# Kernel optimization log

Hardware: AMD Instinct MI355X
Metric: run time of the kernel (lower is better)

## Reference

```python
import jax, jax.numpy as jnp
import numpy as np

D_MODEL = 1024
N_HEADS = 16
D_FF = 2 * D_MODEL
EPS = 1e-6


def setup_inputs() -> dict:
    key = jax.random.key(0)
    ks = jax.random.split(key, 12)
    B, S, D = 2, 2048, D_MODEL
    w = lambda k, shape: (jax.random.normal(k, shape, dtype=jnp.float32) * 0.02)
    return {
        "x": jax.random.normal(ks[0], (B, S, D), dtype=jnp.float32),
        "mask": jnp.ones((B, S, S), dtype=jnp.int32),
        "alpha1": jnp.ones((D,), jnp.float32),
        "bias1": jnp.zeros((D,), jnp.float32),
        "Wq": w(ks[1], (D, D)), "bq": jnp.zeros((D,), jnp.float32),
        "Wk": w(ks[2], (D, D)), "bk": jnp.zeros((D,), jnp.float32),
        "Wv": w(ks[3], (D, D)), "bv": jnp.zeros((D,), jnp.float32),
        "Wo": w(ks[4], (D, D)), "bo": jnp.zeros((D,), jnp.float32),
        "alpha2": jnp.ones((D,), jnp.float32),
        "bias2": jnp.zeros((D,), jnp.float32),
        "W1": w(ks[5], (D, D_FF)), "b1": jnp.zeros((D_FF,), jnp.float32),
        "W2": w(ks[6], (D_FF, D)), "b2": jnp.zeros((D,), jnp.float32),
    }


def _norm(x, alpha, bias):
    # torch: alpha*(x-mean)/(std+eps)+bias, std is unbiased (ddof=1)
    mu = jnp.mean(x, axis=-1, keepdims=True)
    sd = jnp.std(x, axis=-1, ddof=1, keepdims=True)
    return alpha * (x - mu) / (sd + EPS) + bias


def _gelu(x):
    return jax.nn.gelu(x, approximate=False)  # torch F.gelu exact


def _attention(x2, mask, Wq, bq, Wk, bk, Wv, bv, Wo, bo):
    B, S, D = x2.shape
    h, dk = N_HEADS, D // N_HEADS
    # project and split heads: [B, h, S, dk]
    q = (x2 @ Wq + bq).reshape(B, S, h, dk).transpose(0, 2, 1, 3)
    k = (x2 @ Wk + bk).reshape(B, S, h, dk).transpose(0, 2, 1, 3)
    v = (x2 @ Wv + bv).reshape(B, S, h, dk).transpose(0, 2, 1, 3)
    scores = jnp.einsum('bhqd,bhkd->bhqk', q, k) / np.sqrt(dk).astype(np.float32)
    scores = jnp.where(mask[:, None] == 0, jnp.float32(-1e9), scores)
    attn = jax.nn.softmax(scores, axis=-1)
    out = jnp.einsum('bhqk,bhkd->bhqd', attn, v)
    out = out.transpose(0, 2, 1, 3).reshape(B, S, D)
    return out @ Wo + bo


def reference(x, mask, alpha1, bias1, Wq, bq, Wk, bk, Wv, bv, Wo, bo,
              alpha2, bias2, W1, b1, W2, b2):
    x2 = _norm(x, alpha1, bias1)
    x = x + _attention(x2, mask, Wq, bq, Wk, bk, Wv, bv, Wo, bo)
    x2 = _norm(x, alpha2, bias2)
    ff = _gelu(_gelu(x2 @ W1 + b1) @ W2 + b2)
    return x + ff
```

## Files before the change

### kernel.cpp

```cpp
#include <hip/hip_runtime.h>
#include <math.h>

typedef __attribute__((ext_vector_type(8))) short v8s;
typedef __attribute__((ext_vector_type(4))) float v4f;
typedef __attribute__((ext_vector_type(2))) float v2f;
typedef __attribute__((ext_vector_type(16))) float v16f;
typedef __attribute__((ext_vector_type(4))) unsigned int v4u;
typedef __attribute__((ext_vector_type(2))) unsigned int v2u;

#define MFMA16(a,b,c) __builtin_amdgcn_mfma_f32_16x16x32_bf16(a,b,c,0,0,0)
#define MFMA32(a,b,c) __builtin_amdgcn_mfma_f32_32x32x16_bf16(a,b,c,0,0,0)
#define QSCALE 0.18033688011112042f
#define MFIX   12.0f

typedef const __attribute__((address_space(1))) void* gp1_t;
typedef __attribute__((address_space(3))) void* lp3_t;
__device__ __forceinline__ void gll16(const void* g, void* l){
  __builtin_amdgcn_global_load_lds((gp1_t)g, (lp3_t)l, 16, 0, 0);
}
#define VMCNT(n) asm volatile("s_waitcnt vmcnt(" #n ")" ::: "memory")

__device__ __forceinline__ unsigned short f2b(float f){
  unsigned u = __builtin_bit_cast(unsigned, f);
  u += 0x7FFFu + ((u>>16)&1u);
  return (unsigned short)(u>>16);
}
__device__ __forceinline__ float b2f(unsigned short u){
  return __builtin_bit_cast(float, ((unsigned)u)<<16);
}
__device__ __forceinline__ unsigned cvtpk(float lo, float hi){
  unsigned r;
  asm("v_cvt_pk_bf16_f32 %0, %1, %2" : "=v"(r) : "v"(lo), "v"(hi));
  return r;
}
__device__ __forceinline__ float gelu_exact(float x){
  return 0.5f*x*(1.0f + erff(x*0.70710678118654752f));
}

__global__ __launch_bounds__(256) void ln_kernel(const float* __restrict__ x,
    const float* __restrict__ alpha, const float* __restrict__ bias,
    unsigned short* __restrict__ out)
{
  const int D = 1024;
  int row = blockIdx.x;
  int tid = threadIdx.x;
  const float* xr = x + (size_t)row*D;
  v4f v = ((const v4f*)xr)[tid];
  float s  = v[0]+v[1]+v[2]+v[3];
  float s2 = v[0]*v[0]+v[1]*v[1]+v[2]*v[2]+v[3]*v[3];
  #pragma unroll
  for (int off=1; off<64; off<<=1){ s += __shfl_xor(s, off); s2 += __shfl_xor(s2, off); }
  __shared__ float red[8];
  int w = tid>>6;
  if ((tid&63)==0){ red[w]=s; red[4+w]=s2; }
  __syncthreads();
  s  = red[0]+red[1]+red[2]+red[3];
  s2 = red[4]+red[5]+red[6]+red[7];
  float mu  = s*(1.0f/D);
  float var = (s2 - (float)D*mu*mu)*(1.0f/(D-1));
  float inv = 1.0f/(sqrtf(fmaxf(var,0.0f)) + 1e-6f);
  v4f a  = ((const v4f*)alpha)[tid];
  v4f bi = ((const v4f*)bias)[tid];
  unsigned short o[4];
  #pragma unroll
  for (int i=0;i<4;i++) o[i] = f2b(a[i]*(v[i]-mu)*inv + bi[i]);
  v2u pk; pk[0] = (unsigned)o[0] | ((unsigned)o[1]<<16);
          pk[1] = (unsigned)o[2] | ((unsigned)o[3]<<16);
  ((v2u*)(out + (size_t)row*D))[tid] = pk;
}

__global__ __launch_bounds__(256) void preprocess(
    const float* __restrict__ Wq, const float* __restrict__ Wk,
    const float* __restrict__ Wv, const float* __restrict__ Wo,
    const float* __restrict__ W1, const float* __restrict__ W2,
    const int* __restrict__ mask, const float* __restrict__ x,
    const float* __restrict__ alpha1, const float* __restrict__ bias1,
    unsigned short* __restrict__ wqkvT, unsigned short* __restrict__ woT,
    unsigned short* __restrict__ w1T, unsigned short* __restrict__ w2T,
    unsigned char* __restrict__ flags, unsigned short* __restrict__ x2b)
{
  __shared__ float t[32][33];
  __shared__ float red[8];
  __shared__ int f[4];
  int bid = blockIdx.x;
  int tid = threadIdx.x;
  if (bid < 8192){
    const float* in; unsigned short* out; int K, N, idx;
    if (bid < 3072){
      int m = bid >> 10; idx = bid & 1023;
      in = (m==0)?Wq:(m==1)?Wk:Wv; out = wqkvT + (size_t)m*1024*1024; K=1024; N=1024;
    } else if (bid < 4096){ idx = bid-3072; in=Wo; out=woT; K=1024; N=1024; }
    else if (bid < 6144){   idx = bid-4096; in=W1; out=w1T; K=1024; N=2048; }
    else {                  idx = bid-6144; in=W2; out=w2T; K=2048; N=1024; }
    int ntiles = N >> 5;
    int n0 = (idx % ntiles)*32, k0 = (idx / ntiles)*32;
    int tx = tid & 31, ty = tid >> 5;
    #pragma unroll
    for (int j=0;j<4;j++) t[ty+8*j][tx] = in[(size_t)(k0+ty+8*j)*N + n0+tx];
    __syncthreads();
    #pragma unroll
    for (int j=0;j<4;j++) out[(size_t)(n0+ty+8*j)*K + k0+tx] = f2b(t[tx][ty+8*j]);
  } else if (bid < 10240){
    const int S = 2048;
    int idx = bid - 8192;
    int kt = idx & 31, qt = (idx>>5)&31, b = idx>>10;
    const int* mp = mask + (size_t)b*S*S + (size_t)(qt*64)*S + kt*64;
    int ok = 1;
    #pragma unroll
    for (int i=0;i<16;i++){
      int e = tid + i*256;
      int row = e>>6, col = e&63;
      ok &= (mp[(size_t)row*S + col] != 0);
    }
    ok = __all(ok) ? 1 : 0;
    if ((tid&63)==0) f[tid>>6] = ok;
    __syncthreads();
    if (tid==0) flags[idx] = (unsigned char)(f[0]&f[1]&f[2]&f[3]);
  } else {
    const int D = 1024;
    int row = bid - 10240;
    const float* xr = x + (size_t)row*D;
    v4f v = ((const v4f*)xr)[tid];
    float s  = v[0]+v[1]+v[2]+v[3];
    float s2 = v[0]*v[0]+v[1]*v[1]+v[2]*v[2]+v[3]*v[3];
    #pragma unroll
    for (int off=1; off<64; off<<=1){ s += __shfl_xor(s, off); s2 += __shfl_xor(s2, off); }
    int w = tid>>6;
    if ((tid&63)==0){ red[w]=s; red[4+w]=s2; }
    __syncthreads();
    s  = red[0]+red[1]+red[2]+red[3];
    s2 = red[4]+red[5]+red[6]+red[7];
    float mu  = s*(1.0f/D);
    float var = (s2 - (float)D*mu*mu)*(1.0f/(D-1));
    float inv = 1.0f/(sqrtf(fmaxf(var,0.0f)) + 1e-6f);
    v4f a  = ((const v4f*)alpha1)[tid];
    v4f bi = ((const v4f*)bias1)[tid];
    unsigned short o[4];
    #pragma unroll
    for (int i=0;i<4;i++) o[i] = f2b(a[i]*(v[i]-mu)*inv + bi[i]);
    v2u pk; pk[0] = (unsigned)o[0] | ((unsigned)o[1]<<16);
            pk[1] = (unsigned)o[2] | ((unsigned)o[3]<<16);
    ((v2u*)(x2b + (size_t)row*D))[tid] = pk;
  }
}

__global__ __launch_bounds__(256) void gemm_qkv(
    const unsigned short* __restrict__ A, const unsigned short* __restrict__ Bt,
    const float* __restrict__ bq, const float* __restrict__ bk, const float* __restrict__ bv,
    unsigned short* __restrict__ qB, unsigned short* __restrict__ kB,
    unsigned short* __restrict__ vT)
{
  const int K = 1024, N = 1024;
  __shared__ unsigned short As[3][128][32];
  __shared__ unsigned short Bs[3][128][32];
  int m0 = blockIdx.x*128;
  int ny = blockIdx.y;
  int seg = ny>>3;
  int n0g = ny*128;
  int tid = threadIdx.x;
  int w = tid>>6, l = tid&63;
  int wm = (w>>1)*64, wn = (w&1)*64;
  int r16 = l&15, kq = l>>4;
  v4f acc[4][4] = {};
  int t4 = tid>>2, c8 = (tid&3)*8;
  const unsigned short* Ag = A  + (size_t)(m0 + t4)*K + c8;
  const unsigned short* Bg = Bt + (size_t)(n0g + t4)*K + c8;
  auto stageG = [&](int kb, int idx){
    char* a = (char*)&As[idx][0][0] + w*1024;
    char* b = (char*)&Bs[idx][0][0] + w*1024;
    gll16(Ag + kb,                a);
    gll16(Ag + (size_t)64*K + kb, a + 4096);
    gll16(Bg + kb,                b);
    gll16(Bg + (size_t)64*K + kb, b + 4096);
  };
  const int nk = K/32;
  stageG(0, 0); stageG(32, 1);
  for (int i=0; i<nk; i++){
    int cur = i%3;
    if (i+1 < nk) VMCNT(4); else VMCNT(0);
    __builtin_amdgcn_s_barrier();
    if (i+2 < nk) stageG((i+2)*32, (i+2)%3);
    v8s a[4], b[4];
    #pragma unroll
    for (int mi=0;mi<4;mi++) a[mi] = *(const v8s*)&As[cur][wm+mi*16+r16][kq*8];
    #pragma unroll
    for (int ni=0;ni<4;ni++) b[ni] = *(const v8s*)&Bs[cur][wn+ni*16+r16][kq*8];
    #pragma unroll
    for (int mi=0;mi<4;mi++)
      #pragma unroll
      for (int ni=0;ni<4;ni++)
        acc[mi][ni] = MFMA16(a[mi], b[ni], acc[mi][ni]);
  }
  int ncol0 = (ny&7)*128;
  if (seg < 2){
    unsigned short* ob = (seg==0) ? qB : kB;
    const float*    bp = (seg==0) ? bq : bk;
    float sc = (seg==0) ? QSCALE : 1.0f;
    #pragma unroll
    for (int mi=0;mi<4;mi++){
      #pragma unroll
      for (int ni=0;ni<4;ni++){
        int col = ncol0 + wn + ni*16 + r16;
        float bvv = bp[col];
        #pragma unroll
        for (int r=0;r<4;r++){
          int row = m0 + wm + mi*16 + kq*4 + r;
          ob[(size_t)row*N + col] = f2b((acc[mi][ni][r] + bvv)*sc);
        }
      }
    }
  } else {
    #pragma unroll
    for (int mi=0;mi<4;mi++){
      #pragma unroll
      for (int ni=0;ni<4;ni++){
        int col = ncol0 + wn + ni*16 + r16;
        int hh = col >> 6, dk = col & 63;
        float bvv = bv[col];
        int row = m0 + wm + mi*16 + kq*4;
        int bb = row >> 11, s = row & 2047;
        v2u pk;
        pk[0] = cvtpk(acc[mi][ni][0]+bvv, acc[mi][ni][1]+bvv);
        pk[1] = cvtpk(acc[mi][ni][2]+bvv, acc[mi][ni][3]+bvv);
        *(v2u*)(vT + ((size_t)(bb*16+hh)*64 + dk)*2048 + s) = pk;
      }
    }
  }
}

template<int MODE>
__global__ __launch_bounds__(256) void gemm64_bt(
    const unsigned short* __restrict__ A, const unsigned short* __restrict__ Bt,
    const float* __restrict__ bias, const float* __restrict__ res,
    unsigned short* __restrict__ outb, float* __restrict__ outf,
    int M, int N, int K)
{
  __shared__ unsigned short As[3][64][32];
  __shared__ unsigned short Bs[3][128][32];
  int m0 = blockIdx.x*64, n0 = blockIdx.y*128;
  int tid = threadIdx.x;
  int w = tid>>6, l = tid&63;
  int wm = (w>>1)*32, wn = (w&1)*64;
  int r16 = l&15, kq = l>>4;
  v4f acc[2][4] = {};
  int t4 = tid>>2, c8 = (tid&3)*8;
  const unsigned short* Ag = A  + (size_t)(m0 + t4)*K + c8;
  const unsigned short* Bg = Bt + (size_t)(n0 + t4)*K + c8;
  auto stageG = [&](int kb, int idx){
    char* a = (char*)&As[idx][0][0] + w*1024;
    char* b = (char*)&Bs[idx][0][0] + w*1024;
    gll16(Ag + kb,                a);
    gll16(Bg + kb,                b);
    gll16(Bg + (size_t)64*K + kb, b + 4096);
  };
  const int nk = K/32;
  stageG(0, 0); stageG(32, 1);
  for (int i=0; i<nk; i++){
    int cur = i%3;
    if (i+1 < nk) VMCNT(3); else VMCNT(0);
    __builtin_amdgcn_s_barrier();
    if (i+2 < nk) stageG((i+2)*32, (i+2)%3);
    v8s a[2], b[4];
    #pragma unroll
    for (int mi=0;mi<2;mi++) a[mi] = *(const v8s*)&As[cur][wm+mi*16+r16][kq*8];
    #pragma unroll
    for (int ni=0;ni<4;ni++) b[ni] = *(const v8s*)&Bs[cur][wn+ni*16+r16][kq*8];
    #pragma unroll
    for (int mi=0;mi<2;mi++)
      #pragma unroll
      for (int ni=0;ni<4;ni++)
        acc[mi][ni] = MFMA16(a[mi], b[ni], acc[mi][ni]);
  }
  #pragma unroll
  for (int mi=0;mi<2;mi++){
    #pragma unroll
    for (int ni=0;ni<4;ni++){
      int col = n0 + wn + ni*16 + r16;
      float bv = bias[col];
      #pragma unroll
      for (int r=0;r<4;r++){
        int row = m0 + wm + mi*16 + kq*4 + r;
        float t = acc[mi][ni][r] + bv;
        if (MODE==2 || MODE==3) t = gelu_exact(t);
        if (MODE==2) outb[(size_t)row*N + col] = f2b(t);
        else         outf[(size_t)row*N + col] = t + res[(size_t)row*N + col];
      }
    }
  }
}

__global__ __launch_bounds__(256, 4) void attn_kernel(
    const unsigned short* __restrict__ Q, const unsigned short* __restrict__ Kb,
    const unsigned short* __restrict__ vT, const int* __restrict__ mask,
    const unsigned char* __restrict__ flags,
    unsigned short* __restrict__ Opart, float* __restrict__ ml)
{
  const int S = 2048, D = 1024;
  __shared__ unsigned short Kb2[2][64][64];
  __shared__ unsigned short Vb2[2][64][64];
  int bid = (blockIdx.x & 7)*128 + (blockIdx.x >> 3);
  int half = bid & 1;
  int qt = (bid >> 1) & 15;
  int bh = bid >> 5;
  int b = bh >> 4, h = bh & 15;
  int tid = threadIdx.x, w = tid>>6, l = tid&63;
  int l31 = l & 31, hi = l >> 5;
  int pidx = (l ^ 32) << 2;
  const unsigned short* Qp  = Q  + (size_t)b*S*D + h*64;
  const unsigned short* Kp  = Kb + (size_t)b*S*D + h*64;
  const unsigned short* vTp = vT + (size_t)bh*64*S;
  int qrow = qt*128 + w*32 + l31;
  v8s qfr[4];
  #pragma unroll
  for (int ks=0;ks<4;ks++)
    qfr[ks] = *(const v8s*)(Qp + (size_t)qrow*D + ks*16 + hi*8);
  float l_run = 0.0f;
  v16f o0 = {}, o1 = {};
  const int* mp = mask + (size_t)b*S*S;
  const unsigned char* fl = flags + ((size_t)b*32 + qt*2)*32;
  int kt0 = half*16;
  unsigned long long okmask = __ballot( l < 16 ? ((fl[kt0+l] & fl[32+kt0+l]) != 0) : 1 );

  int srow = l>>3;
  int gsw  = (l&7) ^ srow;
  auto stage = [&](int ktg, int idx){
    int kt64 = ktg*64;
    #pragma unroll
    for (int sub=0; sub<2; sub++){
      int row = w*16 + sub*8 + srow;
      gll16(Kp  + (size_t)(kt64+row)*D + gsw*8, &Kb2[idx][w*16+sub*8][0]);
      gll16(vTp + (size_t)row*S + kt64 + gsw*8, &Vb2[idx][w*16+sub*8][0]);
    }
  };
  auto bfrag = [&](unsigned a0, unsigned a1, unsigned a4, unsigned a5) -> v8s {
    unsigned p0 = (unsigned)__builtin_amdgcn_ds_bpermute(pidx, (int)a0);
    unsigned p1 = (unsigned)__builtin_amdgcn_ds_bpermute(pidx, (int)a1);
    unsigned p4 = (unsigned)__builtin_amdgcn_ds_bpermute(pidx, (int)a4);
    unsigned p5 = (unsigned)__builtin_amdgcn_ds_bpermute(pidx, (int)a5);
    v4u pw;
    pw[0] = hi ? p4 : a0;
    pw[1] = hi ? p5 : a1;
    pw[2] = hi ? a4 : p0;
    pw[3] = hi ? a5 : p1;
    return __builtin_bit_cast(v8s, pw);
  };

  stage(kt0, 0);
  int cur = 0;
  for (int it=0; it<16; it++){
    __syncthreads();
    if (it+1 < 16) stage(kt0+it+1, cur^1);
    int ktg = kt0 + it;
    int l7 = l & 7;
    v16f s0 = {}, s1 = {};
    __builtin_amdgcn_s_setprio(1);
    #pragma unroll
    for (int ks=0; ks<4; ks++){
      v8s kf0 = *(const v8s*)&Kb2[cur][l31     ][(((ks*2) + hi) ^ l7)*8];
      v8s kf1 = *(const v8s*)&Kb2[cur][32 + l31][(((ks*2) + hi) ^ l7)*8];
      s0 = MFMA32(kf0, qfr[ks], s0);
      s1 = MFMA32(kf1, qfr[ks], s1);
    }
    __builtin_amdgcn_s_setprio(0);
    if (((~okmask) >> it) & 1ull){
      #pragma unroll
      for (int r=0;r<16;r++){
        int kvl = (r&3) + 8*(r>>2) + 4*hi;
        if (mp[(size_t)qrow*S + ktg*64 + kvl]      == 0) s0[r] = -3.0e38f;
        if (mp[(size_t)qrow*S + ktg*64 + 32 + kvl] == 0) s1[r] = -3.0e38f;
      }
    }
    #pragma unroll
    for (int r=0;r<16;r++){
      s0[r] = exp2f(s0[r] - MFIX);
      s1[r] = exp2f(s1[r] - MFIX);
    }
    float a0 = ((s0[0]+s0[1])+(s0[2]+s0[3])) + ((s0[4]+s0[5])+(s0[6]+s0[7]));
    float a1 = ((s0[8]+s0[9])+(s0[10]+s0[11])) + ((s0[12]+s0[13])+(s0[14]+s0[15]));
    float a2 = ((s1[0]+s1[1])+(s1[2]+s1[3])) + ((s1[4]+s1[5])+(s1[6]+s1[7]));
    float a3 = ((s1[8]+s1[9])+(s1[10]+s1[11])) + ((s1[12]+s1[13])+(s1[14]+s1[15]));
    float rs = (a0+a1) + (a2+a3);
    rs += __shfl_xor(rs, 32);
    l_run += rs;
    v8s pb0 = bfrag(cvtpk(s0[0],s0[1]),  cvtpk(s0[2],s0[3]),
                    cvtpk(s0[4],s0[5]),  cvtpk(s0[6],s0[7]));
    v8s pb1 = bfrag(cvtpk(s0[8],s0[9]),  cvtpk(s0[10],s0[11]),
                    cvtpk(s0[12],s0[13]),cvtpk(s0[14],s0[15]));
    v8s pb2 = bfrag(cvtpk(s1[0],s1[1]),  cvtpk(s1[2],s1[3]),
                    cvtpk(s1[4],s1[5]),  cvtpk(s1[6],s1[7]));
    v8s pb3 = bfrag(cvtpk(s1[8],s1[9]),  cvtpk(s1[10],s1[11]),
                    cvtpk(s1[12],s1[13]),cvtpk(s1[14],s1[15]));
    __builtin_amdgcn_s_setprio(1);
    #pragma unroll
    for (int kvs=0; kvs<4; kvs++){
      v8s pb = (kvs==0) ? pb0 : (kvs==1) ? pb1 : (kvs==2) ? pb2 : pb3;
      v8s vv0 = *(const v8s*)&Vb2[cur][l31     ][(((kvs*2) + hi) ^ l7)*8];
      v8s vv1 = *(const v8s*)&Vb2[cur][32 + l31][(((kvs*2) + hi) ^ l7)*8];
      o0 = MFMA32(vv0, pb, o0);
      o1 = MFMA32(vv1, pb, o1);
    }
    __builtin_amdgcn_s_setprio(0);
    cur ^= 1;
  }
  int rowg = b*S + qrow;
  unsigned short* Op = Opart + (size_t)half*4096*1024 + (size_t)rowg*1024 + h*64;
  #pragma unroll
  for (int p=0; p<8; p++){
    int dk = (p&1)*2 + 8*(p>>1) + 4*hi;
    *(unsigned*)(Op + dk)      = cvtpk(o0[2*p], o0[2*p+1]);
    *(unsigned*)(Op + 32 + dk) = cvtpk(o1[2*p], o1[2*p+1]);
  }
  if (!hi){
    float* mlp = ml + ((size_t)half*4096 + rowg)*32 + h*2;
    mlp[0] = l_run;
  }
}

__global__ __launch_bounds__(256) void attn_combine(const unsigned short* __restrict__ Opart,
    const float* __restrict__ ml, unsigned short* __restrict__ outB)
{
  int row = blockIdx.x;
  int t = threadIdx.x;
  int col = t*4;
  int head = col >> 6;
  float l1 = ml[(size_t)row*32 + head*2];
  float l2 = ml[((size_t)4096 + row)*32 + head*2];
  float inv = 1.0f / (l1 + l2);
  v2u au = *(const v2u*)(Opart + (size_t)row*1024 + col);
  v2u bu = *(const v2u*)(Opart + (size_t)4096*1024 + (size_t)row*1024 + col);
  float a0 = b2f((unsigned short)(au[0]&0xffff)), a1 = b2f((unsigned short)(au[0]>>16));
  float a2 = b2f((unsigned short)(au[1]&0xffff)), a3 = b2f((unsigned short)(au[1]>>16));
  float c0 = b2f((unsigned short)(bu[0]&0xffff)), c1 = b2f((unsigned short)(bu[0]>>16));
  float c2 = b2f((unsigned short)(bu[1]&0xffff)), c3 = b2f((unsigned short)(bu[1]>>16));
  v2u pk;
  pk[0] = cvtpk((a0 + c0)*inv, (a1 + c1)*inv);
  pk[1] = cvtpk((a2 + c2)*inv, (a3 + c3)*inv);
  *(v2u*)(outB + (size_t)row*1024 + col) = pk;
}

extern "C" void kernel_launch(void* const* d_in, const int* in_sizes, int n_in,
                              void* d_out, int out_size, void* d_ws, size_t ws_size,
                              hipStream_t stream)
{
  const int D=1024, DFF=2048, BS=4096;
  const float* x      = (const float*)d_in[0];
  const int*   mask   = (const int*)d_in[1];
  const float* alpha1 = (const float*)d_in[2];
  const float* bias1  = (const float*)d_in[3];
  const float* Wq     = (const float*)d_in[4];
  const float* bq     = (const float*)d_in[5];
  const float* Wk     = (const float*)d_in[6];
  const float* bk     = (const float*)d_in[7];
  const float* Wv     = (const float*)d_in[8];
  const float* bv     = (const float*)d_in[9];
  const float* Wo     = (const float*)d_in[10];
  const float* bo     = (const float*)d_in[11];
  const float* alpha2 = (const float*)d_in[12];
  const float* bias2  = (const float*)d_in[13];
  const float* W1     = (const float*)d_in[14];
  const float* b1     = (const float*)d_in[15];
  const float* W2     = (const float*)d_in[16];
  const float* b2     = (const float*)d_in[17];
  float* outp = (float*)d_out;

  char* ws = (char*)d_ws;
  size_t off = 0;
  auto alloc = [&](size_t bytes){ void* p = ws+off; off += (bytes+255)&~(size_t)255; return p; };
  unsigned short* x2b    = (unsigned short*)alloc((size_t)BS*D*2);
  unsigned short* qB     = (unsigned short*)alloc((size_t)BS*D*2);
  unsigned short* kB     = (unsigned short*)alloc((size_t)BS*D*2);
  unsigned short* vT     = (unsigned short*)alloc((size_t)BS*D*2);
  unsigned short* attnB  = (unsigned short*)alloc((size_t)BS*D*2);
  unsigned short* h1     = (unsigned short*)alloc((size_t)BS*DFF*2);
  float*          xres   = (float*)alloc((size_t)BS*D*4);
  unsigned short* wqkvT  = (unsigned short*)alloc((size_t)3*D*D*2);
  unsigned short* woT    = (unsigned short*)alloc((size_t)D*D*2);
  unsigned short* w1T    = (unsigned short*)alloc((size_t)D*DFF*2);
  unsigned short* w2T    = (unsigned short*)alloc((size_t)DFF*D*2);
  unsigned char*  flg    = (unsigned char*)alloc(2048);
  unsigned short* Opart  = (unsigned short*)alloc((size_t)2*BS*D*2);
  float*          mlbuf  = (float*)alloc((size_t)2*BS*16*2*4);

  preprocess<<<14336, 256, 0, stream>>>(Wq, Wk, Wv, Wo, W1, W2,
                                        mask, x, alpha1, bias1,
                                        wqkvT, woT, w1T, w2T, flg, x2b);

  gemm_qkv<<<dim3(BS/128, 24), 256, 0, stream>>>(x2b, wqkvT, bq, bk, bv, qB, kB, vT);

  attn_kernel<<<1024, 256, 0, stream>>>(qB, kB, vT, mask, flg, Opart, mlbuf);
  attn_combine<<<4096, 256, 0, stream>>>(Opart, mlbuf, attnB);

  gemm64_bt<1><<<dim3(BS/64, D/128), 256, 0, stream>>>(attnB, woT, bo, x, nullptr, xres, BS, D, D);

  ln_kernel<<<BS, 256, 0, stream>>>(xres, alpha2, bias2, x2b);

  gemm64_bt<2><<<dim3(BS/64, DFF/128), 256, 0, stream>>>(x2b, w1T, b1, nullptr, h1, nullptr, BS, DFF, D);
  gemm64_bt<3><<<dim3(BS/64, D/128), 256, 0, stream>>>(h1, w2T, b2, xres, nullptr, outp, BS, D, DFF);
}
```

Before: 249.7 us.

## Add triple-buffered BK=64 GEMM with async LDS loads for Wo and W2

Adds a new GEMM kernel for the two N=1024 output projections (attention Wo and FFN W2). It uses a K-tile of 64, a three-stage shared-memory ring filled by direct global-to-LDS loads, and an XOR swizzle to avoid bank conflicts. The aim is to hide global load latency and reduce barrier count per K step on the memory-bound, lower-occupancy projections. The cost is more LDS per block (about 72KB), which limits how many blocks fit per CU.

After: 238.0 us (median of 2 runs). 1.05x faster.

```diff
diff --git a/kernel.cpp b/kernel.cpp
--- a/kernel.cpp
+++ b/kernel.cpp
@@ -281,9 +281,77 @@
       for (int r=0;r<4;r++){
         int row = m0 + wm + mi*16 + kq*4 + r;
         float t = acc[mi][ni][r] + bv;
-        if (MODE==2 || MODE==3) t = gelu_exact(t);
+        if (MODE==2) t = gelu_exact(t);
         if (MODE==2) outb[(size_t)row*N + col] = f2b(t);
         else         outf[(size_t)row*N + col] = t + res[(size_t)row*N + col];
+      }
+    }
+  }
+}
+
+template<int MODE>
+__global__ __launch_bounds__(256) void gemm64_bk64(
+    const unsigned short* __restrict__ A, const unsigned short* __restrict__ Bt,
+    const float* __restrict__ bias, const float* __restrict__ res,
+    float* __restrict__ outf, int M, int N, int K)
+{
+  __shared__ unsigned short As[3][64][64];
+  __shared__ unsigned short Bs[3][128][64];
+  int m0 = blockIdx.x*64, n0 = blockIdx.y*128;
+  int tid = threadIdx.x;
+  int w = tid>>6, l = tid&63;
+  int wm = (w>>1)*32, wn = (w&1)*64;
+  int r16 = l&15, kq = l>>4;
+  v4f acc[2][4] = {};
+  int srow8 = l>>3;
+  int gsw   = (l&7) ^ srow8;
+  auto stageG = [&](int kb, int idx){
+    #pragma unroll
+    for (int sub=0; sub<2; sub++){
+      int row = w*16 + sub*8 + srow8;
+      gll16(A + (size_t)(m0+row)*K + kb + gsw*8, &As[idx][w*16+sub*8][0]);
+    }
+    #pragma unroll
+    for (int sub=0; sub<4; sub++){
+      int row = w*32 + sub*8 + srow8;
+      gll16(Bt + (size_t)(n0+row)*K + kb + gsw*8, &Bs[idx][w*32+sub*8][0]);
+    }
+  };
+  const int nk = K/64;
+  stageG(0, 0); stageG(64, 1);
+  int rx = r16 & 7;
+  for (int i=0; i<nk; i++){
+    int cur = i%3;
+    if (i+1 < nk) VMCNT(6); else VMCNT(0);
+    __builtin_amdgcn_s_barrier();
+    if (i+2 < nk) stageG((i+2)*64, (i+2)%3);
+    #pragma unroll
+    for (int ks=0; ks<2; ks++){
+      int gl = ((ks*4 + kq) ^ rx)*8;
+      v8s a[2], b[4];
+      #pragma unroll
+      for (int mi=0;mi<2;mi++) a[mi] = *(const v8s*)&As[cur][wm+mi*16+r16][gl];
+      #pragma unroll
+      for (int ni=0;ni<4;ni++) b[ni] = *(const v8s*)&Bs[cur][wn+ni*16+r16][gl];
+      #pragma unroll
+      for (int mi=0;mi<2;mi++)
+        #pragma unroll
+        for (int ni=0;ni<4;ni++)
+          acc[mi][ni] = MFMA16(a[mi], b[ni], acc[mi][ni]);
+    }
+  }
+  #pragma unroll
+  for (int mi=0;mi<2;mi++){
+    #pragma unroll
+    for (int ni=0;ni<4;ni++){
+      int col = n0 + wn + ni*16 + r16;
+      float bv = bias[col];
+      #pragma unroll
+      for (int r=0;r<4;r++){
+        int row = m0 + wm + mi*16 + kq*4 + r;
+        float t = acc[mi][ni][r] + bv;
+        if (MODE==3) t = gelu_exact(t);
+        outf[(size_t)row*N + col] = t + res[(size_t)row*N + col];
       }
     }
   }
@@ -490,10 +558,10 @@
   attn_kernel<<<1024, 256, 0, stream>>>(qB, kB, vT, mask, flg, Opart, mlbuf);
   attn_combine<<<4096, 256, 0, stream>>>(Opart, mlbuf, attnB);
 
-  gemm64_bt<1><<<dim3(BS/64, D/128), 256, 0, stream>>>(attnB, woT, bo, x, nullptr, xres, BS, D, D);
+  gemm64_bk64<1><<<dim3(BS/64, D/128), 256, 0, stream>>>(attnB, woT, bo, x, xres, BS, D, D);
 
   ln_kernel<<<BS, 256, 0, stream>>>(xres, alpha2, bias2, x2b);
 
   gemm64_bt<2><<<dim3(BS/64, DFF/128), 256, 0, stream>>>(x2b, w1T, b1, nullptr, h1, nullptr, BS, DFF, D);
-  gemm64_bt<3><<<dim3(BS/64, D/128), 256, 0, stream>>>(h1, w2T, b2, xres, nullptr, outp, BS, D, DFF);
-}
+  gemm64_bk64<3><<<dim3(BS/64, D/128), 256, 0, stream>>>(h1, w2T, b2, xres, outp, BS, D, DFF);
+}
```
